# Kernel optimization log

Measured on AMD Instinct MI355X. Metric: run time of the kernel, lower is better.

Reference implementation:

```python
import jax, jax.numpy as jnp
import numpy as np

N_NODES = 50000
N_EDGES = 800000
IN_FEAT = 8
H = 128
L = 6
NUM_GRAPHS = 64
EPS_MSG = 1e-7
EPS_SM = 1e-16
LN_EPS = 1e-5


def _ln(x, g, b):
    mu = jnp.mean(x, axis=-1, keepdims=True)
    var = jnp.var(x, axis=-1, keepdims=True)
    return (x - mu) * jax.lax.rsqrt(var + LN_EPS) * g + b


def setup_inputs() -> dict:
    key = jax.random.key(0)
    ks = jax.random.split(key, 12)
    x = jax.random.normal(ks[0], (N_NODES, IN_FEAT), dtype=jnp.float32)
    edge_index = jax.random.randint(ks[1], (2, N_EDGES), 0, N_NODES)
    batch_ids = jnp.sort(jax.random.randint(ks[2], (N_NODES,), 0, NUM_GRAPHS))
    s = 0.05
    return {
        "x": x,
        "edge_index": edge_index,
        "batch_ids": batch_ids,
        "node_W": jax.random.normal(ks[3], (IN_FEAT, H), jnp.float32) * s,
        "node_b": jnp.zeros((H,), jnp.float32),
        "ln_g": jnp.ones((L, H), jnp.float32),
        "ln_b": jnp.zeros((L, H), jnp.float32),
        "t": jnp.ones((L,), jnp.float32),
        "W1": jax.random.normal(ks[4], (L, H, 2 * H), jnp.float32) * s,
        "b1": jnp.zeros((L, 2 * H), jnp.float32),
        "mln_g": jnp.ones((L, 2 * H), jnp.float32),
        "mln_b": jnp.zeros((L, 2 * H), jnp.float32),
        "W2": jax.random.normal(ks[5], (L, 2 * H, H), jnp.float32) * s,
        "b2": jnp.zeros((L, H), jnp.float32),
    }


def reference(x, edge_index, batch_ids, node_W, node_b, ln_g, ln_b, t, W1, b1, mln_g, mln_b, W2, b2):
    src, dst = edge_index[0], edge_index[1]
    n = x.shape[0]
    # node encoder
    x = x @ node_W + node_b  # [N, H]
    for i in range(L):
        # DeepGCNLayer res+: h = relu(LN(x)); x = x + conv(h)
        h = jax.nn.relu(_ln(x, ln_g[i], ln_b[i]))
        # GENConv message: relu(x_j) + eps
        m = jax.nn.relu(h[src]) + EPS_MSG  # [E, H]
        # softmax aggregation over destination segments (temperature t)
        scaled = m * t[i]
        mx = jax.ops.segment_max(scaled, dst, num_segments=n)
        mx = jnp.where(jnp.isfinite(mx), mx, 0.0)
        e = jnp.exp(scaled - mx[dst])
        denom = jax.ops.segment_sum(e, dst, num_segments=n)
        aggr = jax.ops.segment_sum(m * e, dst, num_segments=n) / (denom + EPS_SM)
        # GENConv: out = mlp(aggr + x_r)
        u = aggr + h
        u = u @ W1[i] + b1[i]
        u = jax.nn.relu(_ln(u, mln_g[i], mln_b[i]))
        u = u @ W2[i] + b2[i]
        x = x + u
    # global_add_pool
    return jax.ops.segment_sum(x, batch_ids, num_segments=NUM_GRAPHS)  # [G, H]
```

## Files before the change

kernel.cpp:

```cpp
#include <hip/hip_runtime.h>
#include <hip/hip_bf16.h>
#include <math.h>

#define N_NODES 50000
#define N_EDGES 800000
#define IN_FEAT 8
#define HDIM 128
#define NLAYERS 6
#define NUM_GRAPHS 64
#define EPS_MSG 1e-7f
#define EPS_SM 1e-16f
#define LN_EPS 1e-5f
#define SCAN_NB 49

typedef __attribute__((ext_vector_type(8))) short short8;
typedef __attribute__((ext_vector_type(4))) float floatx4;

__device__ __forceinline__ ushort f2bf(float x) {
    __hip_bfloat16 h = __float2bfloat16(x);
    return *reinterpret_cast<ushort*>(&h);
}
__device__ __forceinline__ float bf2f(ushort u) {
    unsigned int v = ((unsigned int)u) << 16;
    return __uint_as_float(v);
}

__global__ void k_encode_ln(const float* __restrict__ xin, const float* __restrict__ W,
                            const float* __restrict__ bias, const float* __restrict__ g0,
                            const float* __restrict__ b0, float* __restrict__ X,
                            ushort2* __restrict__ Hb) {
    __shared__ float sW[IN_FEAT * HDIM];
    int tid = threadIdx.x;
    int wid = tid >> 6, lane = tid & 63;
    for (int i = tid; i < IN_FEAT * HDIM; i += 256) sW[i] = W[i];
    __syncthreads();
    int n = blockIdx.x * 4 + wid;
    if (n >= N_NODES) return;
    int c0 = 2 * lane, c1 = 2 * lane + 1;
    float a0 = bias[c0], a1 = bias[c1];
#pragma unroll
    for (int f = 0; f < IN_FEAT; ++f) {
        float xf = xin[n * IN_FEAT + f];
        a0 += xf * sW[f * HDIM + c0];
        a1 += xf * sW[f * HDIM + c1];
    }
    float2 xv; xv.x = a0; xv.y = a1;
    *(float2*)(X + (size_t)n * HDIM + c0) = xv;
    float s = a0 + a1, sq = a0 * a0 + a1 * a1;
#pragma unroll
    for (int off = 32; off; off >>= 1) {
        s += __shfl_xor(s, off, 64);
        sq += __shfl_xor(sq, off, 64);
    }
    float mean = s * (1.f / 128.f);
    float var = sq * (1.f / 128.f) - mean * mean;
    float inv = rsqrtf(var + LN_EPS);
    float h0 = (a0 - mean) * inv * g0[c0] + b0[c0];
    float h1 = (a1 - mean) * inv * g0[c1] + b0[c1];
    ushort2 o;
    o.x = f2bf(fmaxf(h0, 0.f));
    o.y = f2bf(fmaxf(h1, 0.f));
    Hb[(size_t)n * 64 + lane] = o;
}

__global__ void k_hist(const int* __restrict__ dst, int* __restrict__ deg) {
    int i = blockIdx.x * blockDim.x + threadIdx.x;
    if (i < N_EDGES) atomicAdd(&deg[dst[i]], 1);
}

__global__ void k_bsum(const int* __restrict__ deg, int* __restrict__ bsum) {
    int i = blockIdx.x * 1024 + threadIdx.x;
    int v = (i < N_NODES) ? deg[i] : 0;
#pragma unroll
    for (int off = 32; off; off >>= 1) v += __shfl_xor(v, off, 64);
    __shared__ int wsum[16];
    int wid = threadIdx.x >> 6;
    if ((threadIdx.x & 63) == 0) wsum[wid] = v;
    __syncthreads();
    if (threadIdx.x < 16) {
        int s = wsum[threadIdx.x];
#pragma unroll
        for (int off = 8; off; off >>= 1) s += __shfl_xor(s, off, 16);
        if (threadIdx.x == 0) bsum[blockIdx.x] = s;
    }
}

__global__ void k_scan_small(int* __restrict__ bsum) {
    int lane = threadIdx.x;
    int orig = (lane < SCAN_NB) ? bsum[lane] : 0;
    int v = orig;
#pragma unroll
    for (int off = 1; off < 64; off <<= 1) {
        int u = __shfl_up(v, off, 64);
        if (lane >= off) v += u;
    }
    if (lane < SCAN_NB) bsum[lane] = v - orig;
}

__global__ void k_scan_final(const int* __restrict__ deg, const int* __restrict__ bsum,
                             int* __restrict__ row_ptr, int* __restrict__ cursor) {
    __shared__ int wsum[16];
    int i = blockIdx.x * 1024 + threadIdx.x;
    int t = threadIdx.x;
    int lane = t & 63, wid = t >> 6;
    int orig = (i < N_NODES) ? deg[i] : 0;
    int v = orig;
#pragma unroll
    for (int off = 1; off < 64; off <<= 1) {
        int u = __shfl_up(v, off, 64);
        if (lane >= off) v += u;
    }
    if (lane == 63) wsum[wid] = v;
    __syncthreads();
    if (t < 16) {
        int s = wsum[t];
#pragma unroll
        for (int off = 1; off < 16; off <<= 1) {
            int u = __shfl_up(s, off, 16);
            if (t >= off) s += u;
        }
        wsum[t] = s;
    }
    __syncthreads();
    int base = bsum[blockIdx.x] + (wid ? wsum[wid - 1] : 0);
    int excl = base + v - orig;
    if (i < N_NODES) {
        row_ptr[i] = excl;
        cursor[i] = excl;
    }
    if (i == 0) row_ptr[N_NODES] = N_EDGES;
}

__global__ void k_scatter(const int* __restrict__ src, const int* __restrict__ dst,
                          int* __restrict__ cursor, int* __restrict__ csr_src) {
    int i = blockIdx.x * blockDim.x + threadIdx.x;
    if (i < N_EDGES) {
        int pos = atomicAdd(&cursor[dst[i]], 1);
        csr_src[pos] = src[i];
    }
}

__global__ void k_prep(const float* __restrict__ W1, const float* __restrict__ W2,
                       ushort* __restrict__ Wp1, ushort* __restrict__ Wp2) {
    int idx = blockIdx.x * 256 + threadIdx.x;
    if (idx < 24576) {
        int lane = idx & 63;
        int frag = idx >> 6;
        int cf = frag & 15, kb = (frag >> 4) & 3, l = frag >> 6;
        const float* Wl = W1 + (size_t)l * 128 * 256;
        ushort* o = Wp1 + (size_t)idx * 8;
        int k0 = kb * 32 + (lane >> 4) * 8;
        int c = cf * 16 + (lane & 15);
#pragma unroll
        for (int j = 0; j < 8; ++j) o[j] = f2bf(Wl[(k0 + j) * 256 + c]);
    } else if (idx < 49152) {
        int i2 = idx - 24576;
        int lane = i2 & 63;
        int frag = i2 >> 6;
        int cf = frag & 7, kb = (frag >> 3) & 7, l = frag >> 6;
        const float* Wl = W2 + (size_t)l * 256 * 128;
        ushort* o = Wp2 + (size_t)i2 * 8;
        int k0 = kb * 32 + (lane >> 4) * 8;
        int c = cf * 16 + (lane & 15);
#pragma unroll
        for (int j = 0; j < 8; ++j) o[j] = f2bf(Wl[(k0 + j) * 128 + c]);
    }
}

__global__ void k_aggr(const ushort2* __restrict__ Hh, const int* __restrict__ row_ptr,
                       const int* __restrict__ csr, const float* __restrict__ t_all,
                       int layer, ushort2* __restrict__ U) {
    int wid = threadIdx.x >> 6;
    int lane = threadIdx.x & 63;
    int n = blockIdx.x * 4 + wid;
    if (n >= N_NODES) return;
    float tt = t_all[layer];
    int beg = row_ptr[n], end = row_ptr[n + 1];
    int cnt = end - beg;
    float den0 = 0.f, den1 = 0.f, num0 = 0.f, num1 = 0.f;

    auto proc = [&](ushort2 c) {
        float m0 = bf2f(c.x) + EPS_MSG;
        float m1 = bf2f(c.y) + EPS_MSG;
        float e0 = __expf(m0 * tt);
        float e1 = __expf(m1 * tt);
        den0 += e0; num0 += m0 * e0;
        den1 += e1; num1 += m1 * e1;
    };
    auto LDI = [&](int k) -> ushort2 {
        int kk = (k < cnt) ? k : cnt - 1;
        return Hh[(size_t)csr[beg + kk] * 64 + lane];
    };

    if (cnt > 0) {
        ushort2 p0 = LDI(0), p1 = LDI(1), p2 = LDI(2), p3 = LDI(3),
                p4 = LDI(4), p5 = LDI(5), p6 = LDI(6), p7 = LDI(7);
        int e = 0;
        while (e + 8 <= cnt) {
            ushort2 c0 = p0, c1 = p1, c2 = p2, c3 = p3,
                    c4 = p4, c5 = p5, c6 = p6, c7 = p7;
            p0 = LDI(e + 8);  p1 = LDI(e + 9);  p2 = LDI(e + 10); p3 = LDI(e + 11);
            p4 = LDI(e + 12); p5 = LDI(e + 13); p6 = LDI(e + 14); p7 = LDI(e + 15);
            proc(c0); proc(c1); proc(c2); proc(c3);
            proc(c4); proc(c5); proc(c6); proc(c7);
            e += 8;
        }
        int rem = cnt - e;
        if (rem > 0) proc(p0);
        if (rem > 1) proc(p1);
        if (rem > 2) proc(p2);
        if (rem > 3) proc(p3);
        if (rem > 4) proc(p4);
        if (rem > 5) proc(p5);
        if (rem > 6) proc(p6);
    }

    float a0 = num0 / (den0 + EPS_SM);
    float a1 = num1 / (den1 + EPS_SM);
    ushort2 hs = Hh[(size_t)n * 64 + lane];
    ushort2 o;
    o.x = f2bf(a0 + bf2f(hs.x));
    o.y = f2bf(a1 + bf2f(hs.y));
    U[(size_t)n * 64 + lane] = o;
}

__global__ __launch_bounds__(256) void k_mlp_fused(
    const ushort* __restrict__ U, float* __restrict__ X,
    const short8* __restrict__ Wp1, const short8* __restrict__ Wp2,
    const float* __restrict__ b1, const float* __restrict__ mg,
    const float* __restrict__ mb, const float* __restrict__ b2,
    const float* __restrict__ nlg, const float* __restrict__ nlb,
    ushort* __restrict__ HbOut, int writeHb) {
    __shared__ ushort sBuf[64 * 264];
    __shared__ float sStat[4][64][2];
    __shared__ float sMV[64][2];
    int tid = threadIdx.x;
    int w = tid >> 6, lane = tid & 63;
    int g = lane >> 4, c15 = lane & 15;
    int n0 = blockIdx.x * 64;

#pragma unroll
    for (int i = 0; i < 4; ++i) {
        int id = tid + i * 256;
        int row = id >> 4, cc = id & 15;
        int n = n0 + row;
        short8 v = {0, 0, 0, 0, 0, 0, 0, 0};
        if (n < N_NODES) v = *(const short8*)(U + (size_t)n * 128 + cc * 8);
        *(short8*)(sBuf + row * 136 + cc * 8) = v;
    }
    __syncthreads();

    floatx4 acc1[4][4];
#pragma unroll
    for (int rf = 0; rf < 4; ++rf)
#pragma unroll
        for (int cf = 0; cf < 4; ++cf) acc1[rf][cf] = (floatx4){0.f, 0.f, 0.f, 0.f};

#pragma unroll
    for (int kb = 0; kb < 4; ++kb) {
        short8 bfr[4];
#pragma unroll
        for (int cf = 0; cf < 4; ++cf) bfr[cf] = Wp1[(kb * 16 + w * 4 + cf) * 64 + lane];
        short8 af[4];
#pragma unroll
        for (int rf = 0; rf < 4; ++rf)
            af[rf] = *(const short8*)(sBuf + (rf * 16 + c15) * 136 + kb * 32 + g * 8);
#pragma unroll
        for (int rf = 0; rf < 4; ++rf)
#pragma unroll
            for (int cf = 0; cf < 4; ++cf)
                acc1[rf][cf] = __builtin_amdgcn_mfma_f32_16x16x32_bf16(af[rf], bfr[cf], acc1[rf][cf], 0, 0, 0);
    }

    int colb = w * 64;
    float bv[4], gv[4], bbv[4];
#pragma unroll
    for (int cf = 0; cf < 4; ++cf) {
        int c = colb + cf * 16 + c15;
        bv[cf] = b1[c]; gv[cf] = mg[c]; bbv[cf] = mb[c];
    }
    float sS[4][4], sQ[4][4];
#pragma unroll
    for (int rf = 0; rf < 4; ++rf)
#pragma unroll
        for (int reg = 0; reg < 4; ++reg) {
            float s = 0.f, q = 0.f;
#pragma unroll
            for (int cf = 0; cf < 4; ++cf) {
                float v = acc1[rf][cf][reg] + bv[cf];
                acc1[rf][cf][reg] = v;
                s += v; q += v * v;
            }
            sS[rf][reg] = s; sQ[rf][reg] = q;
        }
#pragma unroll
    for (int off = 1; off < 16; off <<= 1)
#pragma unroll
        for (int rf = 0; rf < 4; ++rf)
#pragma unroll
            for (int reg = 0; reg < 4; ++reg) {
                sS[rf][reg] += __shfl_xor(sS[rf][reg], off, 64);
                sQ[rf][reg] += __shfl_xor(sQ[rf][reg], off, 64);
            }
    if (c15 == 0) {
#pragma unroll
        for (int rf = 0; rf < 4; ++rf)
#pragma unroll
            for (int reg = 0; reg < 4; ++reg) {
                int row = rf * 16 + g * 4 + reg;
                sStat[w][row][0] = sS[rf][reg];
                sStat[w][row][1] = sQ[rf][reg];
            }
    }
    __syncthreads();
    if (tid < 64) {
        float s = sStat[0][tid][0] + sStat[1][tid][0] + sStat[2][tid][0] + sStat[3][tid][0];
        float q = sStat[0][tid][1] + sStat[1][tid][1] + sStat[2][tid][1] + sStat[3][tid][1];
        float mean = s * (1.f / 256.f);
        float var = q * (1.f / 256.f) - mean * mean;
        sMV[tid][0] = mean;
        sMV[tid][1] = rsqrtf(var + LN_EPS);
    }
    __syncthreads();

#pragma unroll
    for (int rf = 0; rf < 4; ++rf)
#pragma unroll
        for (int reg = 0; reg < 4; ++reg) {
            int row = rf * 16 + g * 4 + reg;
            float mean = sMV[row][0], inv = sMV[row][1];
#pragma unroll
            for (int cf = 0; cf < 4; ++cf) {
                float v = (acc1[rf][cf][reg] - mean) * inv * gv[cf] + bbv[cf];
                sBuf[row * 264 + colb + cf * 16 + c15] = f2bf(fmaxf(v, 0.f));
            }
        }
    __syncthreads();

    floatx4 acc2[4][2];
#pragma unroll
    for (int rf = 0; rf < 4; ++rf) {
        acc2[rf][0] = (floatx4){0.f, 0.f, 0.f, 0.f};
        acc2[rf][1] = (floatx4){0.f, 0.f, 0.f, 0.f};
    }
#pragma unroll
    for (int kb = 0; kb < 8; ++kb) {
        short8 bfr[2];
#pragma unroll
        for (int cf = 0; cf < 2; ++cf) bfr[cf] = Wp2[(kb * 8 + w * 2 + cf) * 64 + lane];
        short8 af[4];
#pragma unroll
        for (int rf = 0; rf < 4; ++rf)
            af[rf] = *(const short8*)(sBuf + (rf * 16 + c15) * 264 + kb * 32 + g * 8);
#pragma unroll
        for (int rf = 0; rf < 4; ++rf)
#pragma unroll
            for (int cf = 0; cf < 2; ++cf)
                acc2[rf][cf] = __builtin_amdgcn_mfma_f32_16x16x32_bf16(af[rf], bfr[cf], acc2[rf][cf], 0, 0, 0);
    }

    float b2v[2];
    b2v[0] = b2[w * 32 + c15];
    b2v[1] = b2[w * 32 + 16 + c15];
    float gn[2] = {0.f, 0.f}, bn[2] = {0.f, 0.f};
    if (writeHb) {
        gn[0] = nlg[w * 32 + c15];      bn[0] = nlb[w * 32 + c15];
        gn[1] = nlg[w * 32 + 16 + c15]; bn[1] = nlb[w * 32 + 16 + c15];
    }
#pragma unroll
    for (int rf = 0; rf < 4; ++rf)
#pragma unroll
        for (int reg = 0; reg < 4; ++reg) {
            int row = rf * 16 + g * 4 + reg;
            int n = n0 + row;
            float s = 0.f, q = 0.f;
#pragma unroll
            for (int cf = 0; cf < 2; ++cf) {
                float xold = (n < N_NODES) ? X[(size_t)n * 128 + w * 32 + cf * 16 + c15] : 0.f;
                float v = xold + acc2[rf][cf][reg] + b2v[cf];
                acc2[rf][cf][reg] = v;
                s += v; q += v * v;
            }
            if (writeHb) {
#pragma unroll
                for (int off = 1; off < 16; off <<= 1) {
                    s += __shfl_xor(s, off, 64);
                    q += __shfl_xor(q, off, 64);
                }
                if (c15 == 0) {
                    sStat[w][row][0] = s;
                    sStat[w][row][1] = q;
                }
            }
        }
    if (writeHb) {
        __syncthreads();
        if (tid < 64) {
            float s = sStat[0][tid][0] + sStat[1][tid][0] + sStat[2][tid][0] + sStat[3][tid][0];
            float q = sStat[0][tid][1] + sStat[1][tid][1] + sStat[2][tid][1] + sStat[3][tid][1];
            float mean = s * (1.f / 128.f);
            float var = q * (1.f / 128.f) - mean * mean;
            sMV[tid][0] = mean;
            sMV[tid][1] = rsqrtf(var + LN_EPS);
        }
        __syncthreads();
    }
#pragma unroll
    for (int rf = 0; rf < 4; ++rf)
#pragma unroll
        for (int reg = 0; reg < 4; ++reg) {
            int row = rf * 16 + g * 4 + reg;
            int n = n0 + row;
            if (n < N_NODES) {
                float mean = 0.f, inv = 0.f;
                if (writeHb) { mean = sMV[row][0]; inv = sMV[row][1]; }
#pragma unroll
                for (int cf = 0; cf < 2; ++cf) {
                    int col = w * 32 + cf * 16 + c15;
                    float v = acc2[rf][cf][reg];
                    X[(size_t)n * 128 + col] = v;
                    if (writeHb) {
                        float h = (v - mean) * inv * gn[cf] + bn[cf];
                        HbOut[(size_t)n * 128 + col] = f2bf(fmaxf(h, 0.f));
                    }
                }
            }
        }
}

__global__ void k_pool(const float* __restrict__ X, const int* __restrict__ batch,
                       float* __restrict__ out) {
    __shared__ int sBat[128];
    int c = threadIdx.x;
    int n0 = blockIdx.x * 128;
    int nend = n0 + 128; if (nend > N_NODES) nend = N_NODES;
    sBat[c] = (n0 + c < N_NODES) ? batch[n0 + c] : -1;
    __syncthreads();
    float acc = 0.f;
    int cur = sBat[0];
    for (int n = n0; n < nend; ++n) {
        int g = sBat[n - n0];
        if (g != cur) {
            atomicAdd(&out[cur * HDIM + c], acc);
            acc = 0.f;
            cur = g;
        }
        acc += X[(size_t)n * HDIM + c];
    }
    if (nend > n0) atomicAdd(&out[cur * HDIM + c], acc);
}

extern "C" void kernel_launch(void* const* d_in, const int* in_sizes, int n_in,
                              void* d_out, int out_size, void* d_ws, size_t ws_size,
                              hipStream_t stream) {
    const float* x_in   = (const float*)d_in[0];
    const int*   eidx   = (const int*)d_in[1];
    const int*   batch  = (const int*)d_in[2];
    const float* node_W = (const float*)d_in[3];
    const float* node_b = (const float*)d_in[4];
    const float* ln_g   = (const float*)d_in[5];
    const float* ln_b   = (const float*)d_in[6];
    const float* t_all  = (const float*)d_in[7];
    const float* W1     = (const float*)d_in[8];
    const float* b1     = (const float*)d_in[9];
    const float* mg     = (const float*)d_in[10];
    const float* mb     = (const float*)d_in[11];
    const float* W2     = (const float*)d_in[12];
    const float* b2     = (const float*)d_in[13];
    float* out = (float*)d_out;

    char* ws = (char*)d_ws;
    float*  X   = (float*)(ws + 0);
    ushort2* Hb = (ushort2*)(ws + 25600000);
    ushort2* U  = (ushort2*)(ws + 38400000);
    ushort* Wp1 = (ushort*)(ws + 51200000);
    ushort* Wp2 = (ushort*)(ws + 51600000);
    int* deg     = (int*)(ws + 52000000);
    int* row_ptr = (int*)(ws + 52200064);
    int* cursor  = (int*)(ws + 52400128);
    int* csr_src = (int*)(ws + 52600192);
    int* bsum    = (int*)(ws + 55800192);

    const int* e_src = eidx;
    const int* e_dst = eidx + N_EDGES;

    hipMemsetAsync(deg, 0, N_NODES * sizeof(int), stream);
    k_hist<<<(N_EDGES + 255) / 256, 256, 0, stream>>>(e_dst, deg);
    k_bsum<<<SCAN_NB, 1024, 0, stream>>>(deg, bsum);
    k_scan_small<<<1, 64, 0, stream>>>(bsum);
    k_scan_final<<<SCAN_NB, 1024, 0, stream>>>(deg, bsum, row_ptr, cursor);
    k_scatter<<<(N_EDGES + 255) / 256, 256, 0, stream>>>(e_src, e_dst, cursor, csr_src);
    k_prep<<<192, 256, 0, stream>>>(W1, W2, Wp1, Wp2);
    k_encode_ln<<<12500, 256, 0, stream>>>(x_in, node_W, node_b, ln_g, ln_b, X, Hb);

    for (int l = 0; l < NLAYERS; ++l) {
        k_aggr<<<12500, 256, 0, stream>>>(Hb, row_ptr, csr_src, t_all, l, U);
        int wh = (l < NLAYERS - 1) ? 1 : 0;
        const float* nlg = ln_g + (wh ? (l + 1) : 0) * HDIM;
        const float* nlb = ln_b + (wh ? (l + 1) : 0) * HDIM;
        k_mlp_fused<<<(N_NODES + 63) / 64, 256, 0, stream>>>(
            (const ushort*)U, X,
            (const short8*)(Wp1 + (size_t)l * 32768), (const short8*)(Wp2 + (size_t)l * 32768),
            b1 + l * 256, mg + l * 256, mb + l * 256, b2 + l * 128,
            nlg, nlb, (ushort*)Hb, wh);
    }

    hipMemsetAsync(out, 0, NUM_GRAPHS * HDIM * sizeof(float), stream);
    k_pool<<<(N_NODES + 127) / 128, 128, 0, stream>>>(X, batch, out);
}
```

Measured before the change: 634.9 us.

## Split edge aggregation across two waves per node and bucket CSR scatter

The aggregation kernel now assigns two wavefronts to each destination node. Each wave handles alternate edges, and the partial numerators and denominators are combined through shared memory. This doubles memory-level parallelism for the gather-heavy softmax aggregation, at the cost of a block barrier and half the nodes per block. CSR construction also adds a coarse bucketing pass by dst>>6 before the per-node scatter, to improve atomic and write locality. The price is an extra pass over the edges and a 6.4 MB temporary buffer.

Measured after the change: 1.020 ms. 60.6% more time.

```diff
diff --git a/kernel.cpp b/kernel.cpp
--- a/kernel.cpp
+++ b/kernel.cpp
@@ -12,6 +12,7 @@
 #define EPS_SM 1e-16f
 #define LN_EPS 1e-5f
 #define SCAN_NB 49
+#define NBUCK 782
 
 typedef __attribute__((ext_vector_type(8))) short short8;
 typedef __attribute__((ext_vector_type(4))) float floatx4;
@@ -63,9 +64,14 @@
     Hb[(size_t)n * 64 + lane] = o;
 }
 
-__global__ void k_hist(const int* __restrict__ dst, int* __restrict__ deg) {
+__global__ void k_hist(const int* __restrict__ dst, int* __restrict__ deg,
+                       int* __restrict__ bhist) {
     int i = blockIdx.x * blockDim.x + threadIdx.x;
-    if (i < N_EDGES) atomicAdd(&deg[dst[i]], 1);
+    if (i < N_EDGES) {
+        int d = dst[i];
+        atomicAdd(&deg[d], 1);
+        atomicAdd(&bhist[d >> 6], 1);
+    }
 }
 
 __global__ void k_bsum(const int* __restrict__ deg, int* __restrict__ bsum) {
@@ -131,12 +137,52 @@
     if (i == 0) row_ptr[N_NODES] = N_EDGES;
 }
 
-__global__ void k_scatter(const int* __restrict__ src, const int* __restrict__ dst,
-                          int* __restrict__ cursor, int* __restrict__ csr_src) {
+__global__ void k_bscan(const int* __restrict__ bhist, int* __restrict__ bcur) {
+    __shared__ int wsum[16];
+    int t = threadIdx.x;
+    int lane = t & 63, wid = t >> 6;
+    int orig = (t < NBUCK) ? bhist[t] : 0;
+    int v = orig;
+#pragma unroll
+    for (int off = 1; off < 64; off <<= 1) {
+        int u = __shfl_up(v, off, 64);
+        if (lane >= off) v += u;
+    }
+    if (lane == 63) wsum[wid] = v;
+    __syncthreads();
+    if (t < 16) {
+        int s = wsum[t];
+#pragma unroll
+        for (int off = 1; off < 16; off <<= 1) {
+            int u = __shfl_up(s, off, 16);
+            if (t >= off) s += u;
+        }
+        wsum[t] = s;
+    }
+    __syncthreads();
+    int excl = (wid ? wsum[wid - 1] : 0) + v - orig;
+    if (t < NBUCK) bcur[t] = excl;
+}
+
+__global__ void k_bucket(const int* __restrict__ src, const int* __restrict__ dst,
+                         int* __restrict__ bcur, unsigned long long* __restrict__ tmp) {
     int i = blockIdx.x * blockDim.x + threadIdx.x;
     if (i < N_EDGES) {
-        int pos = atomicAdd(&cursor[dst[i]], 1);
-        csr_src[pos] = src[i];
+        int s = src[i], d = dst[i];
+        int pos = atomicAdd(&bcur[d >> 6], 1);
+        tmp[pos] = (((unsigned long long)(unsigned)d) << 32) | (unsigned)s;
+    }
+}
+
+__global__ void k_scatter2(const unsigned long long* __restrict__ tmp,
+                           int* __restrict__ cursor, int* __restrict__ csr_src) {
+    int i = blockIdx.x * blockDim.x + threadIdx.x;
+    if (i < N_EDGES) {
+        unsigned long long v = tmp[i];
+        int d = (int)(v >> 32);
+        int s = (int)(v & 0xffffffffu);
+        int pos = atomicAdd(&cursor[d], 1);
+        csr_src[pos] = s;
     }
 }
 
@@ -167,17 +213,23 @@
     }
 }
 
-__global__ void k_aggr(const ushort2* __restrict__ Hh, const int* __restrict__ row_ptr,
-                       const int* __restrict__ csr, const float* __restrict__ t_all,
-                       int layer, ushort2* __restrict__ U) {
-    int wid = threadIdx.x >> 6;
-    int lane = threadIdx.x & 63;
-    int n = blockIdx.x * 4 + wid;
-    if (n >= N_NODES) return;
+__global__ __launch_bounds__(256) void k_aggr(const ushort2* __restrict__ Hh,
+                                              const int* __restrict__ row_ptr,
+                                              const int* __restrict__ csr,
+                                              const float* __restrict__ t_all,
+                                              int layer, ushort2* __restrict__ U) {
+    __shared__ float part[2][64][4];
+    int tid = threadIdx.x;
+    int wid = tid >> 6, lane = tid & 63;
+    int local = wid >> 1;
+    int half = wid & 1;
+    int n = blockIdx.x * 2 + local;
     float tt = t_all[layer];
     int beg = row_ptr[n], end = row_ptr[n + 1];
     int cnt = end - beg;
+    int mycnt = (cnt - half + 1) >> 1;
     float den0 = 0.f, den1 = 0.f, num0 = 0.f, num1 = 0.f;
+    unsigned laneoff = (unsigned)(lane << 2);
 
     auto proc = [&](ushort2 c) {
         float m0 = bf2f(c.x) + EPS_MSG;
@@ -188,15 +240,16 @@
         den1 += e1; num1 += m1 * e1;
     };
     auto LDI = [&](int k) -> ushort2 {
-        int kk = (k < cnt) ? k : cnt - 1;
-        return Hh[(size_t)csr[beg + kk] * 64 + lane];
+        int kk = (k < mycnt) ? k : mycnt - 1;
+        int sidx = csr[beg + half + 2 * kk];
+        return *(const ushort2*)((const char*)Hh + (((unsigned)sidx << 8) + laneoff));
     };
 
-    if (cnt > 0) {
+    if (mycnt > 0) {
         ushort2 p0 = LDI(0), p1 = LDI(1), p2 = LDI(2), p3 = LDI(3),
                 p4 = LDI(4), p5 = LDI(5), p6 = LDI(6), p7 = LDI(7);
         int e = 0;
-        while (e + 8 <= cnt) {
+        while (e + 8 <= mycnt) {
             ushort2 c0 = p0, c1 = p1, c2 = p2, c3 = p3,
                     c4 = p4, c5 = p5, c6 = p6, c7 = p7;
             p0 = LDI(e + 8);  p1 = LDI(e + 9);  p2 = LDI(e + 10); p3 = LDI(e + 11);
@@ -205,7 +258,7 @@
             proc(c4); proc(c5); proc(c6); proc(c7);
             e += 8;
         }
-        int rem = cnt - e;
+        int rem = mycnt - e;
         if (rem > 0) proc(p0);
         if (rem > 1) proc(p1);
         if (rem > 2) proc(p2);
@@ -215,13 +268,26 @@
         if (rem > 6) proc(p6);
     }
 
-    float a0 = num0 / (den0 + EPS_SM);
-    float a1 = num1 / (den1 + EPS_SM);
-    ushort2 hs = Hh[(size_t)n * 64 + lane];
-    ushort2 o;
-    o.x = f2bf(a0 + bf2f(hs.x));
-    o.y = f2bf(a1 + bf2f(hs.y));
-    U[(size_t)n * 64 + lane] = o;
+    if (half == 1) {
+        part[local][lane][0] = num0;
+        part[local][lane][1] = num1;
+        part[local][lane][2] = den0;
+        part[local][lane][3] = den1;
+    }
+    __syncthreads();
+    if (half == 0) {
+        num0 += part[local][lane][0];
+        num1 += part[local][lane][1];
+        den0 += part[local][lane][2];
+        den1 += part[local][lane][3];
+        float a0 = num0 / (den0 + EPS_SM);
+        float a1 = num1 / (den1 + EPS_SM);
+        ushort2 hs = Hh[(size_t)n * 64 + lane];
+        ushort2 o;
+        o.x = f2bf(a0 + bf2f(hs.x));
+        o.y = f2bf(a1 + bf2f(hs.y));
+        U[(size_t)n * 64 + lane] = o;
+    }
 }
 
 __global__ __launch_bounds__(256) void k_mlp_fused(
@@ -480,21 +546,27 @@
     int* cursor  = (int*)(ws + 52400128);
     int* csr_src = (int*)(ws + 52600192);
     int* bsum    = (int*)(ws + 55800192);
+    int* bhist   = (int*)(ws + 55800448);
+    int* bcur    = (int*)(ws + 55803584);
+    unsigned long long* tmp = (unsigned long long*)(ws + 55806720);
 
     const int* e_src = eidx;
     const int* e_dst = eidx + N_EDGES;
 
     hipMemsetAsync(deg, 0, N_NODES * sizeof(int), stream);
-    k_hist<<<(N_EDGES + 255) / 256, 256, 0, stream>>>(e_dst, deg);
+    hipMemsetAsync(bhist, 0, NBUCK * sizeof(int), stream);
+    k_hist<<<(N_EDGES + 255) / 256, 256, 0, stream>>>(e_dst, deg, bhist);
     k_bsum<<<SCAN_NB, 1024, 0, stream>>>(deg, bsum);
     k_scan_small<<<1, 64, 0, stream>>>(bsum);
     k_scan_final<<<SCAN_NB, 1024, 0, stream>>>(deg, bsum, row_ptr, cursor);
-    k_scatter<<<(N_EDGES + 255) / 256, 256, 0, stream>>>(e_src, e_dst, cursor, csr_src);
+    k_bscan<<<1, 1024, 0, stream>>>(bhist, bcur);
+    k_bucket<<<(N_EDGES + 255) / 256, 256, 0, stream>>>(e_src, e_dst, bcur, tmp);
+    k_scatter2<<<(N_EDGES + 255) / 256, 256, 0, stream>>>(tmp, cursor, csr_src);
     k_prep<<<192, 256, 0, stream>>>(W1, W2, Wp1, Wp2);
     k_encode_ln<<<12500, 256, 0, stream>>>(x_in, node_W, node_b, ln_g, ln_b, X, Hb);
 
     for (int l = 0; l < NLAYERS; ++l) {
-        k_aggr<<<12500, 256, 0, stream>>>(Hb, row_ptr, csr_src, t_all, l, U);
+        k_aggr<<<25000, 256, 0, stream>>>(Hb, row_ptr, csr_src, t_all, l, U);
         int wh = (l < NLAYERS - 1) ? 1 : 0;
         const float* nlg = ln_g + (wh ? (l + 1) : 0) * HDIM;
         const float* nlb = ln_b + (wh ? (l + 1) : 0) * HDIM;
```

## Process two edges per wavefront with 8-byte gathers and 16-bit CSR indices

Applied to the files above, without the earlier changes.

The softmax aggregation kernel now splits each wavefront into two halves. Each half gathers a different neighbor edge, and each lane loads 4 bf16 features (8 bytes) instead of 2. The two halves' partial sums are combined with a cross-half shuffle before the write. CSR source indices are stored as ushort, since the node count fits in 16 bits, and exp is computed as exp2f with a pre-scaled temperature. The aim is more gathers in flight and less index traffic. In exchange it adds masking overhead for odd edge counts and only half the lanes do the final store.

Measured after the change: 805.0 us. 1.27x slower.

```diff
diff --git a/kernel.cpp b/kernel.cpp
--- a/kernel.cpp
+++ b/kernel.cpp
@@ -15,6 +15,7 @@
 
 typedef __attribute__((ext_vector_type(8))) short short8;
 typedef __attribute__((ext_vector_type(4))) float floatx4;
+typedef __attribute__((ext_vector_type(4))) unsigned short ushort4v;
 
 __device__ __forceinline__ ushort f2bf(float x) {
     __hip_bfloat16 h = __float2bfloat16(x);
@@ -132,11 +133,11 @@
 }
 
 __global__ void k_scatter(const int* __restrict__ src, const int* __restrict__ dst,
-                          int* __restrict__ cursor, int* __restrict__ csr_src) {
+                          int* __restrict__ cursor, ushort* __restrict__ csr_src) {
     int i = blockIdx.x * blockDim.x + threadIdx.x;
     if (i < N_EDGES) {
         int pos = atomicAdd(&cursor[dst[i]], 1);
-        csr_src[pos] = src[i];
+        csr_src[pos] = (ushort)src[i];
     }
 }
 
@@ -167,61 +168,91 @@
     }
 }
 
-__global__ void k_aggr(const ushort2* __restrict__ Hh, const int* __restrict__ row_ptr,
-                       const int* __restrict__ csr, const float* __restrict__ t_all,
-                       int layer, ushort2* __restrict__ U) {
-    int wid = threadIdx.x >> 6;
-    int lane = threadIdx.x & 63;
+__global__ __launch_bounds__(256) void k_aggr(const ushort* __restrict__ Hh,
+                                              const int* __restrict__ row_ptr,
+                                              const ushort* __restrict__ csr,
+                                              const float* __restrict__ t_all,
+                                              int layer, ushort* __restrict__ U) {
+    int tid = threadIdx.x;
+    int wid = tid >> 6, lane = tid & 63;
     int n = blockIdx.x * 4 + wid;
-    if (n >= N_NODES) return;
-    float tt = t_all[layer];
-    int beg = row_ptr[n], end = row_ptr[n + 1];
-    int cnt = end - beg;
-    float den0 = 0.f, den1 = 0.f, num0 = 0.f, num1 = 0.f;
-
-    auto proc = [&](ushort2 c) {
-        float m0 = bf2f(c.x) + EPS_MSG;
-        float m1 = bf2f(c.y) + EPS_MSG;
-        float e0 = __expf(m0 * tt);
-        float e1 = __expf(m1 * tt);
-        den0 += e0; num0 += m0 * e0;
-        den1 += e1; num1 += m1 * e1;
+    float ts = t_all[layer] * 1.44269504f;
+    int beg = row_ptr[n], cnt = row_ptr[n + 1] - beg;
+    int h = lane >> 5, l32 = lane & 31;
+    unsigned boff = (unsigned)(l32 << 3);
+    float num0 = 0.f, num1 = 0.f, num2 = 0.f, num3 = 0.f;
+    float den0 = 0.f, den1 = 0.f, den2 = 0.f, den3 = 0.f;
+    int npairs = (cnt + 1) >> 1;
+    int emax = beg + cnt - 1;
+
+    auto LDI = [&](int p) -> ushort4v {
+        int e = beg + 2 * p + h;
+        e = (e < emax) ? e : emax;
+        int sidx = (int)csr[e];
+        return *(const ushort4v*)((const char*)Hh + (((size_t)(unsigned)sidx) << 8) + boff);
     };
-    auto LDI = [&](int k) -> ushort2 {
-        int kk = (k < cnt) ? k : cnt - 1;
-        return Hh[(size_t)csr[beg + kk] * 64 + lane];
+    auto proc = [&](ushort4v v, int p) {
+        float vm = (2 * p + h < cnt) ? 1.f : 0.f;
+        float m0 = bf2f(v.x) + EPS_MSG, m1 = bf2f(v.y) + EPS_MSG;
+        float m2 = bf2f(v.z) + EPS_MSG, m3 = bf2f(v.w) + EPS_MSG;
+        float e0 = exp2f(m0 * ts) * vm, e1 = exp2f(m1 * ts) * vm;
+        float e2 = exp2f(m2 * ts) * vm, e3 = exp2f(m3 * ts) * vm;
+        den0 += e0; num0 = fmaf(m0, e0, num0);
+        den1 += e1; num1 = fmaf(m1, e1, num1);
+        den2 += e2; num2 = fmaf(m2, e2, num2);
+        den3 += e3; num3 = fmaf(m3, e3, num3);
     };
 
     if (cnt > 0) {
-        ushort2 p0 = LDI(0), p1 = LDI(1), p2 = LDI(2), p3 = LDI(3),
-                p4 = LDI(4), p5 = LDI(5), p6 = LDI(6), p7 = LDI(7);
-        int e = 0;
-        while (e + 8 <= cnt) {
-            ushort2 c0 = p0, c1 = p1, c2 = p2, c3 = p3,
-                    c4 = p4, c5 = p5, c6 = p6, c7 = p7;
-            p0 = LDI(e + 8);  p1 = LDI(e + 9);  p2 = LDI(e + 10); p3 = LDI(e + 11);
-            p4 = LDI(e + 12); p5 = LDI(e + 13); p6 = LDI(e + 14); p7 = LDI(e + 15);
-            proc(c0); proc(c1); proc(c2); proc(c3);
-            proc(c4); proc(c5); proc(c6); proc(c7);
-            e += 8;
-        }
-        int rem = cnt - e;
-        if (rem > 0) proc(p0);
-        if (rem > 1) proc(p1);
-        if (rem > 2) proc(p2);
-        if (rem > 3) proc(p3);
-        if (rem > 4) proc(p4);
-        if (rem > 5) proc(p5);
-        if (rem > 6) proc(p6);
-    }
-
-    float a0 = num0 / (den0 + EPS_SM);
-    float a1 = num1 / (den1 + EPS_SM);
-    ushort2 hs = Hh[(size_t)n * 64 + lane];
-    ushort2 o;
-    o.x = f2bf(a0 + bf2f(hs.x));
-    o.y = f2bf(a1 + bf2f(hs.y));
-    U[(size_t)n * 64 + lane] = o;
+        ushort4v p0, p1, p2, p3, p4, p5, p6, p7;
+        p0 = LDI(0);
+        if (npairs > 1) p1 = LDI(1);
+        if (npairs > 2) p2 = LDI(2);
+        if (npairs > 3) p3 = LDI(3);
+        if (npairs > 4) p4 = LDI(4);
+        if (npairs > 5) p5 = LDI(5);
+        if (npairs > 6) p6 = LDI(6);
+        if (npairs > 7) p7 = LDI(7);
+        int p = 0;
+        while (p + 8 <= npairs) {
+            ushort4v c0 = p0, c1 = p1, c2 = p2, c3 = p3,
+                     c4 = p4, c5 = p5, c6 = p6, c7 = p7;
+            if (p + 8 < npairs)  p0 = LDI(p + 8);
+            if (p + 9 < npairs)  p1 = LDI(p + 9);
+            if (p + 10 < npairs) p2 = LDI(p + 10);
+            if (p + 11 < npairs) p3 = LDI(p + 11);
+            if (p + 12 < npairs) p4 = LDI(p + 12);
+            if (p + 13 < npairs) p5 = LDI(p + 13);
+            if (p + 14 < npairs) p6 = LDI(p + 14);
+            if (p + 15 < npairs) p7 = LDI(p + 15);
+            proc(c0, p); proc(c1, p + 1); proc(c2, p + 2); proc(c3, p + 3);
+            proc(c4, p + 4); proc(c5, p + 5); proc(c6, p + 6); proc(c7, p + 7);
+            p += 8;
+        }
+        int rem = npairs - p;
+        if (rem > 0) proc(p0, p);
+        if (rem > 1) proc(p1, p + 1);
+        if (rem > 2) proc(p2, p + 2);
+        if (rem > 3) proc(p3, p + 3);
+        if (rem > 4) proc(p4, p + 4);
+        if (rem > 5) proc(p5, p + 5);
+        if (rem > 6) proc(p6, p + 6);
+    }
+
+    num0 += __shfl_xor(num0, 32, 64); den0 += __shfl_xor(den0, 32, 64);
+    num1 += __shfl_xor(num1, 32, 64); den1 += __shfl_xor(den1, 32, 64);
+    num2 += __shfl_xor(num2, 32, 64); den2 += __shfl_xor(den2, 32, 64);
+    num3 += __shfl_xor(num3, 32, 64); den3 += __shfl_xor(den3, 32, 64);
+
+    if (h == 0) {
+        ushort4v hv = *(const ushort4v*)((const char*)Hh + (((size_t)n) << 8) + boff);
+        ushort4v o;
+        o.x = f2bf(num0 / (den0 + EPS_SM) + bf2f(hv.x));
+        o.y = f2bf(num1 / (den1 + EPS_SM) + bf2f(hv.y));
+        o.z = f2bf(num2 / (den2 + EPS_SM) + bf2f(hv.z));
+        o.w = f2bf(num3 / (den3 + EPS_SM) + bf2f(hv.w));
+        *(ushort4v*)((char*)U + (((size_t)n) << 8) + boff) = o;
+    }
 }
 
 __global__ __launch_bounds__(256) void k_mlp_fused(
@@ -478,8 +509,8 @@
     int* deg     = (int*)(ws + 52000000);
     int* row_ptr = (int*)(ws + 52200064);
     int* cursor  = (int*)(ws + 52400128);
-    int* csr_src = (int*)(ws + 52600192);
-    int* bsum    = (int*)(ws + 55800192);
+    ushort* csr_src = (ushort*)(ws + 52600192);
+    int* bsum    = (int*)(ws + 54400192);
 
     const int* e_src = eidx;
     const int* e_dst = eidx + N_EDGES;
@@ -494,7 +525,8 @@
     k_encode_ln<<<12500, 256, 0, stream>>>(x_in, node_W, node_b, ln_g, ln_b, X, Hb);
 
     for (int l = 0; l < NLAYERS; ++l) {
-        k_aggr<<<12500, 256, 0, stream>>>(Hb, row_ptr, csr_src, t_all, l, U);
+        k_aggr<<<12500, 256, 0, stream>>>((const ushort*)Hb, row_ptr, csr_src, t_all, l,
+                                          (ushort*)U);
         int wh = (l < NLAYERS - 1) ? 1 : 0;
         const float* nlg = ln_g + (wh ? (l + 1) : 0) * HDIM;
         const float* nlb = ln_b + (wh ? (l + 1) : 0) * HDIM;
```
